# Kernel optimization log

Hardware: AMD Instinct MI355X
Metric: run time of the kernel (lower is better)

Reference implementation:

```python
import jax, jax.numpy as jnp
import numpy as np

E = 1024   # embed_dim
H = 16     # num_heads
D = E // H # head_dim
B = 2
S = 2048
YAT_EPS = 0.1


def setup_inputs() -> dict:
    key = jax.random.key(0)
    ks = jax.random.split(key, 5)
    w_scale = (6.0 / (E + E)) ** 0.5  # xavier_uniform bound
    def xavier(k):
        return jax.random.uniform(k, (E, E), jnp.float32, -w_scale, w_scale)
    return {
        "x": jax.random.normal(ks[0], (B, S, E), jnp.float32),
        "Wq": xavier(ks[1]), "bq": jnp.zeros((E,), jnp.float32),
        "Wk": xavier(ks[2]), "bk": jnp.zeros((E,), jnp.float32),
        "Wv": xavier(ks[3]), "bv": jnp.zeros((E,), jnp.float32),
        "Wo": xavier(ks[4]), "bo": jnp.zeros((E,), jnp.float32),
    }


def reference(x, Wq, bq, Wk, bk, Wv, bv, Wo, bo):
    b, s, _ = x.shape
    # Projections (Linear: x @ W + b, flax kernel layout [in, out])
    Q = x @ Wq + bq
    K = x @ Wk + bk
    V = x @ Wv + bv
    # [B, H, S, D]
    Q = Q.reshape(b, s, H, D).transpose(0, 2, 1, 3)
    K = K.reshape(b, s, H, D).transpose(0, 2, 1, 3)
    V = V.reshape(b, s, H, D).transpose(0, 2, 1, 3)
    # L2 normalize along head_dim
    Qn = Q / (jnp.linalg.norm(Q, axis=-1, keepdims=True) + 1e-8)
    Kn = K / (jnp.linalg.norm(K, axis=-1, keepdims=True) + 1e-8)
    # Yat kernel scores: (1 + <q,k>)^2 / (eps + (1 - <q,k>))
    dot = jnp.einsum("bhqd,bhkd->bhqk", Qn, Kn)
    scores = (1.0 + dot) ** 2 / (YAT_EPS + (1.0 - dot))
    # Sum-normalize (no softmax)
    attn = scores / (jnp.sum(scores, axis=-1, keepdims=True) + 1e-6)
    out = jnp.einsum("bhqk,bhkd->bhqd", attn, V)
    out = out.transpose(0, 2, 1, 3).reshape(b, s, E)
    return out @ Wo + bo
```

## Files before the change

### kernel.cpp

```cpp
#include <hip/hip_runtime.h>
#include <math.h>

#define EDIM 1024
#define NH   16
#define HD   64
#define BATCH 2
#define SEQ  2048
#define NROW (BATCH*SEQ)
#define YAT_EPS 0.1f

typedef _Float16 f16;
typedef _Float16 f16x8 __attribute__((ext_vector_type(8)));
typedef _Float16 f16x4 __attribute__((ext_vector_type(4)));
typedef float    f32x4 __attribute__((ext_vector_type(4)));

#define GLL16(gp, lp) __builtin_amdgcn_global_load_lds( \
    (const __attribute__((address_space(1))) void*)(gp), \
    (__attribute__((address_space(3))) void*)(lp), 16, 0, 0)

__global__ __launch_bounds__(256)
void cast_f16_kernel(const float* __restrict__ src, f16* __restrict__ dst)
{
    const int i = (blockIdx.x * 256 + threadIdx.x) * 4;
    const float4 v = *(const float4*)(src + i);
    f16x4 o = {(f16)v.x, (f16)v.y, (f16)v.z, (f16)v.w};
    *(f16x4*)(dst + i) = o;
}

__global__ __launch_bounds__(256)
void transcast_kernel(const float* __restrict__ W, f16* __restrict__ Wt)
{
    __shared__ float T[32][33];
    const int t = threadIdx.x;
    const int r = t >> 3, c4 = (t & 7) * 4;
    const int bi = blockIdx.x * 32, bj = blockIdx.y * 32;
    const float4 v = *(const float4*)(W + (size_t)(bi + r) * 1024 + bj + c4);
    T[r][c4 + 0] = v.x; T[r][c4 + 1] = v.y; T[r][c4 + 2] = v.z; T[r][c4 + 3] = v.w;
    __syncthreads();
    f16x4 o = {(f16)T[c4 + 0][r], (f16)T[c4 + 1][r], (f16)T[c4 + 2][r], (f16)T[c4 + 3][r]};
    *(f16x4*)(Wt + (size_t)(bj + r) * 1024 + bi + c4) = o;
}

__global__ __launch_bounds__(256)
void gemm_f16(const f16* __restrict__ A,
              const f16* __restrict__ B0, const f16* __restrict__ B1, const f16* __restrict__ B2,
              const float* __restrict__ bi0, const float* __restrict__ bi1, const float* __restrict__ bi2,
              void* __restrict__ o0, void* __restrict__ o1, void* __restrict__ o2,
              int e0, int e1, int e2)
{
    __shared__ __align__(16) f16 As[128 * 64];
    __shared__ __align__(16) f16 Bs[128 * 64];

    const int z = blockIdx.z;
    const f16*   Bt   = (z == 0) ? B0  : (z == 1) ? B1  : B2;
    const float* bias = (z == 0) ? bi0 : (z == 1) ? bi1 : bi2;
    void*        Cout = (z == 0) ? o0  : (z == 1) ? o1  : o2;
    const int    epi  = (z == 0) ? e0  : (z == 1) ? e1  : e2;

    const int tid  = threadIdx.x;
    const int lane = tid & 63;
    const int w    = tid >> 6;
    const int cl   = lane & 15;
    const int quad = lane >> 4;
    const int wm = w & 1, wn = w >> 1;
    const int bm = blockIdx.x * 128, bn = blockIdx.y * 128;

    const int srow = w * 8 + (lane >> 3);
    const int scs  = (lane & 7) ^ (lane >> 3);
    const f16* gA = A  + (size_t)(bm + srow) * 1024 + scs * 8;
    const f16* gB = Bt + (size_t)(bn + srow) * 1024 + scs * 8;
    f16* lA = As + w * 512;
    f16* lB = Bs + w * 512;

    f32x4 acc[4][4];
#pragma unroll
    for (int i = 0; i < 4; ++i)
#pragma unroll
        for (int j = 0; j < 4; ++j) acc[i][j] = (f32x4){0.f, 0.f, 0.f, 0.f};

    for (int k0 = 0; k0 < 1024; k0 += 64) {
        __syncthreads();
#pragma unroll
        for (int it = 0; it < 4; ++it) {
            GLL16(gA + (size_t)it * 32 * 1024 + k0, lA + it * 2048);
            GLL16(gB + (size_t)it * 32 * 1024 + k0, lB + it * 2048);
        }
        __syncthreads();
#pragma unroll
        for (int kb = 0; kb < 2; ++kb) {
            f16x8 af[4], bf[4];
#pragma unroll
            for (int mt = 0; mt < 4; ++mt)
                af[mt] = *(const f16x8*)(&As[(wm * 64 + mt * 16 + cl) * 64 +
                                             (((kb * 4 + quad) ^ (cl & 7)) * 8)]);
#pragma unroll
            for (int nt = 0; nt < 4; ++nt)
                bf[nt] = *(const f16x8*)(&Bs[(wn * 64 + nt * 16 + cl) * 64 +
                                             (((kb * 4 + quad) ^ (cl & 7)) * 8)]);
#pragma unroll
            for (int mt = 0; mt < 4; ++mt)
#pragma unroll
                for (int nt = 0; nt < 4; ++nt)
                    acc[mt][nt] = __builtin_amdgcn_mfma_f32_16x16x32_f16(af[mt], bf[nt], acc[mt][nt], 0, 0, 0);
        }
    }

    float bcol[4];
#pragma unroll
    for (int nt = 0; nt < 4; ++nt) bcol[nt] = bias[bn + wn * 64 + nt * 16 + cl];
#pragma unroll
    for (int mt = 0; mt < 4; ++mt)
#pragma unroll
        for (int nt = 0; nt < 4; ++nt)
#pragma unroll
            for (int rg = 0; rg < 4; ++rg) acc[mt][nt][rg] += bcol[nt];

    if (epi == 0) {
        float* C = (float*)Cout;
#pragma unroll
        for (int mt = 0; mt < 4; ++mt)
#pragma unroll
            for (int rg = 0; rg < 4; ++rg) {
                const int row = bm + wm * 64 + mt * 16 + quad * 4 + rg;
#pragma unroll
                for (int nt = 0; nt < 4; ++nt)
                    C[(size_t)row * EDIM + bn + wn * 64 + nt * 16 + cl] = acc[mt][nt][rg];
            }
    } else if (epi == 1) {
        f16* C = (f16*)Cout;
#pragma unroll
        for (int mt = 0; mt < 4; ++mt)
#pragma unroll
            for (int rg = 0; rg < 4; ++rg) {
                float ss = 0.f;
#pragma unroll
                for (int nt = 0; nt < 4; ++nt) ss += acc[mt][nt][rg] * acc[mt][nt][rg];
                ss += __shfl_xor(ss, 1); ss += __shfl_xor(ss, 2);
                ss += __shfl_xor(ss, 4); ss += __shfl_xor(ss, 8);
                const float inv = 1.0f / (sqrtf(ss) + 1e-8f);
                const int row = bm + wm * 64 + mt * 16 + quad * 4 + rg;
                const int b = row >> 11, s = row & (SEQ - 1);
#pragma unroll
                for (int nt = 0; nt < 4; ++nt) {
                    const int col = bn + wn * 64 + nt * 16 + cl;
                    const int h = col >> 6, d = col & 63;
                    C[((size_t)(b * NH + h) * SEQ + s) * HD + d] = (f16)(acc[mt][nt][rg] * inv);
                }
            }
    } else {
        f16* C = (f16*)Cout;
#pragma unroll
        for (int mt = 0; mt < 4; ++mt) {
            const int s0 = bm + wm * 64 + mt * 16 + quad * 4;
            const int b = s0 >> 11, sl = s0 & (SEQ - 1);
#pragma unroll
            for (int nt = 0; nt < 4; ++nt) {
                const int col = bn + wn * 64 + nt * 16 + cl;
                const int h = col >> 6, d = col & 63;
                f16x4 o = {(f16)acc[mt][nt][0], (f16)acc[mt][nt][1],
                           (f16)acc[mt][nt][2], (f16)acc[mt][nt][3]};
                *(f16x4*)(C + ((size_t)(b * NH + h) * HD + d) * SEQ + sl) = o;
            }
        }
    }
}

__global__ __launch_bounds__(256)
void yat_attn(const f16* __restrict__ Qh, const f16* __restrict__ Kh,
              const f16* __restrict__ Vt, f16* __restrict__ AO)
{
    __shared__ __align__(16) char lds[53248];
    f16* KsB = (f16*)(lds + 20480);
    f16* VsB = (f16*)(lds + 36864);

    const int tid  = threadIdx.x;
    const int lane = tid & 63;
    const int w    = tid >> 6;
    const int cl   = lane & 15;
    const int quad = lane >> 4;
    const int wm = w & 1;
    const int wk = w >> 1;
    const int q0 = blockIdx.x * 128;
    const int bh = blockIdx.y;

    const f16* Qg = Qh + (size_t)bh * SEQ * HD;
    const f16* Kg = Kh + (size_t)bh * SEQ * HD;
    const f16* Vg = Vt + (size_t)bh * HD * SEQ;

    const int g8   = lane >> 3;
    const int scs  = (lane & 7) ^ g8;
    const int qrow = w * 8 + g8;
    const int krow = w * 16 + g8;

    {
        const f16* gQ = Qg + (size_t)(q0 + qrow) * HD + scs * 8;
        f16* lQ = (f16*)lds + w * 512;
#pragma unroll
        for (int it = 0; it < 4; ++it)
            GLL16(gQ + it * 32 * HD, lQ + it * 2048);
    }
    __syncthreads();
    f16x8 qf[4][2];
#pragma unroll
    for (int qt = 0; qt < 4; ++qt)
#pragma unroll
        for (int kb = 0; kb < 2; ++kb)
            qf[qt][kb] = *(const f16x8*)((f16*)lds + (wm * 64 + qt * 16 + cl) * 64 +
                                         ((kb * 4 + quad) ^ (cl & 7)) * 8);
    __syncthreads();

    f16* Pw = (f16*)(lds + w * 5120);

    f32x4 O[4][4];
    float rs[4] = {0.f, 0.f, 0.f, 0.f};
#pragma unroll
    for (int i = 0; i < 4; ++i)
#pragma unroll
        for (int j = 0; j < 4; ++j) O[i][j] = (f32x4){0.f, 0.f, 0.f, 0.f};

    const f16* gK = Kg + (size_t)krow * HD + scs * 8;
    const f16* gV = Vg + (size_t)krow * SEQ + scs * 8;
    f16* lK = KsB + w * 1024;
    f16* lV = VsB + w * 1024;

#pragma unroll
    for (int it = 0; it < 2; ++it) {
        GLL16(gK + (size_t)(it * 8) * HD, lK + it * 512);
        GLL16(gV + (size_t)(it * 8) * SEQ, lV + it * 512);
    }

    for (int t0 = 0; t0 < SEQ; t0 += 64) {
        const int buf = (t0 >> 6) & 1;
        __syncthreads();

        if (t0 + 64 < SEQ) {
            const int nb = buf ^ 1;
#pragma unroll
            for (int it = 0; it < 2; ++it) {
                GLL16(gK + (size_t)(t0 + 64 + it * 8) * HD, lK + nb * 4096 + it * 512);
                GLL16(gV + (size_t)(it * 8) * SEQ + t0 + 64, lV + nb * 4096 + it * 512);
            }
        }

        const f16* Ks = KsB + buf * 4096;
        const f16* Vs = VsB + buf * 4096;

        f32x4 s[2][4];
#pragma unroll
        for (int kt = 0; kt < 2; ++kt)
#pragma unroll
            for (int qt = 0; qt < 4; ++qt) s[kt][qt] = (f32x4){0.f, 0.f, 0.f, 0.f};
#pragma unroll
        for (int kb = 0; kb < 2; ++kb) {
            const int sw = ((kb * 4 + quad) ^ (cl & 7)) * 8;
            f16x8 af0 = *(const f16x8*)(&Ks[(wk * 32 +  0 + cl) * 64 + sw]);
            f16x8 af1 = *(const f16x8*)(&Ks[(wk * 32 + 16 + cl) * 64 + sw]);
#pragma unroll
            for (int qt = 0; qt < 4; ++qt) {
                s[0][qt] = __builtin_amdgcn_mfma_f32_16x16x32_f16(af0, qf[qt][kb], s[0][qt], 0, 0, 0);
                s[1][qt] = __builtin_amdgcn_mfma_f32_16x16x32_f16(af1, qf[qt][kb], s[1][qt], 0, 0, 0);
            }
        }

#pragma unroll
        for (int kt = 0; kt < 2; ++kt)
#pragma unroll
            for (int qt = 0; qt < 4; ++qt) {
                f16x4 pk;
                float psum = 0.f;
#pragma unroll
                for (int rg = 0; rg < 4; ++rg) {
                    const float u = (1.0f + YAT_EPS) - s[kt][qt][rg];
                    const float p = fmaf(4.41f, __builtin_amdgcn_rcpf(u), u - 4.2f);
                    psum += p;
                    pk[rg] = (f16)p;
                }
                rs[qt] += psum;
                *(f16x4*)(&Pw[(qt * 16 + cl) * 40 + kt * 16 + quad * 4]) = pk;
            }

        f16x8 pa[4];
#pragma unroll
        for (int qt = 0; qt < 4; ++qt)
            pa[qt] = *(const f16x8*)(&Pw[(qt * 16 + cl) * 40 + quad * 8]);
#pragma unroll
        for (int dn = 0; dn < 4; ++dn) {
            f16x8 vb = *(const f16x8*)(&Vs[(dn * 16 + cl) * 64 +
                                           ((wk * 4 + quad) ^ (cl & 7)) * 8]);
#pragma unroll
            for (int qt = 0; qt < 4; ++qt)
                O[qt][dn] = __builtin_amdgcn_mfma_f32_16x16x32_f16(pa[qt], vb, O[qt][dn], 0, 0, 0);
        }
    }

    __syncthreads();
    float* rs_s = (float*)lds;
    float* Ox   = (float*)(lds + 20480);

#pragma unroll
    for (int qt = 0; qt < 4; ++qt) {
        float t = rs[qt];
        t += __shfl_xor(t, 16);
        t += __shfl_xor(t, 32);
        if (quad == 0) rs_s[wk * 128 + wm * 64 + qt * 16 + cl] = t;
    }
    if (wk == 1) {
#pragma unroll
        for (int qt = 0; qt < 4; ++qt)
#pragma unroll
            for (int dn = 0; dn < 4; ++dn)
#pragma unroll
                for (int rg = 0; rg < 4; ++rg)
                    Ox[(wm * 64 + qt * 16 + quad * 4 + rg) * 64 + dn * 16 + cl] = O[qt][dn][rg];
    }
    __syncthreads();
    if (wk == 0) {
        const int b = bh >> 4, h = bh & 15;
#pragma unroll
        for (int qt = 0; qt < 4; ++qt)
#pragma unroll
            for (int rg = 0; rg < 4; ++rg) {
                const int ql = wm * 64 + qt * 16 + quad * 4 + rg;
                const float tot = rs_s[ql] + rs_s[128 + ql];
                const float inv = 1.0f / (tot + 1e-6f);
                const size_t rowoff = ((size_t)b * SEQ + q0 + ql) * EDIM + h * 64;
#pragma unroll
                for (int dn = 0; dn < 4; ++dn)
                    AO[rowoff + dn * 16 + cl] =
                        (f16)((O[qt][dn][rg] + Ox[ql * 64 + dn * 16 + cl]) * inv);
            }
    }
}

extern "C" void kernel_launch(void* const* d_in, const int* in_sizes, int n_in,
                              void* d_out, int out_size, void* d_ws, size_t ws_size,
                              hipStream_t stream)
{
    const float* x  = (const float*)d_in[0];
    const float* Wq = (const float*)d_in[1];
    const float* bq = (const float*)d_in[2];
    const float* Wk = (const float*)d_in[3];
    const float* bk = (const float*)d_in[4];
    const float* Wv = (const float*)d_in[5];
    const float* bv = (const float*)d_in[6];
    const float* Wo = (const float*)d_in[7];
    const float* bo = (const float*)d_in[8];

    char* p = (char*)d_ws;
    f16* xb  = (f16*)p;                 p += (size_t)NROW * EDIM * 2;
    f16* Wqt = (f16*)p;                 p += (size_t)EDIM * EDIM * 2;
    f16* Wkt = (f16*)p;                 p += (size_t)EDIM * EDIM * 2;
    f16* Wvt = (f16*)p;                 p += (size_t)EDIM * EDIM * 2;
    f16* Wot = (f16*)p;                 p += (size_t)EDIM * EDIM * 2;
    f16* Qhb = (f16*)p;                 p += (size_t)NROW * EDIM * 2;
    f16* Khb = (f16*)p;                 p += (size_t)NROW * EDIM * 2;
    f16* Vtb = (f16*)p;                 p += (size_t)NROW * EDIM * 2;
    f16* AOb = (f16*)p;                 p += (size_t)NROW * EDIM * 2;

    cast_f16_kernel<<<NROW * EDIM / 1024, 256, 0, stream>>>(x, xb);
    transcast_kernel<<<dim3(32, 32), 256, 0, stream>>>(Wq, Wqt);
    transcast_kernel<<<dim3(32, 32), 256, 0, stream>>>(Wk, Wkt);
    transcast_kernel<<<dim3(32, 32), 256, 0, stream>>>(Wv, Wvt);
    transcast_kernel<<<dim3(32, 32), 256, 0, stream>>>(Wo, Wot);

    gemm_f16<<<dim3(NROW / 128, EDIM / 128, 3), 256, 0, stream>>>(
        xb, Wqt, Wkt, Wvt, bq, bk, bv, Qhb, Khb, Vtb, 1, 1, 2);

    yat_attn<<<dim3(SEQ / 128, BATCH * NH), 256, 0, stream>>>(Qhb, Khb, Vtb, AOb);

    gemm_f16<<<dim3(NROW / 128, EDIM / 128, 1), 256, 0, stream>>>(
        AOb, Wot, Wot, Wot, bo, bo, bo, d_out, d_out, d_out, 0, 0, 0);
}
```

Before: 210.7 us.

## Double-buffer GEMM with 64x128 tiles, LDS-staged epilogue stores, merged weight transposes

```diff
diff --git a/kernel.cpp b/kernel.cpp
--- a/kernel.cpp
+++ b/kernel.cpp
@@ -28,8 +28,15 @@
 }
 
 __global__ __launch_bounds__(256)
-void transcast_kernel(const float* __restrict__ W, f16* __restrict__ Wt)
+void transcast4_kernel(const float* __restrict__ W0, const float* __restrict__ W1,
+                       const float* __restrict__ W2, const float* __restrict__ W3,
+                       f16* __restrict__ T0, f16* __restrict__ T1,
+                       f16* __restrict__ T2, f16* __restrict__ T3)
 {
+    const int z = blockIdx.z;
+    const float* W = (z == 0) ? W0 : (z == 1) ? W1 : (z == 2) ? W2 : W3;
+    f16*         Wt = (z == 0) ? T0 : (z == 1) ? T1 : (z == 2) ? T2 : T3;
+
     __shared__ float T[32][33];
     const int t = threadIdx.x;
     const int r = t >> 3, c4 = (t & 7) * 4;
@@ -48,8 +55,7 @@
               void* __restrict__ o0, void* __restrict__ o1, void* __restrict__ o2,
               int e0, int e1, int e2)
 {
-    __shared__ __align__(16) f16 As[128 * 64];
-    __shared__ __align__(16) f16 Bs[128 * 64];
+    __shared__ __align__(16) char lds[24576];
 
     const int z = blockIdx.z;
     const f16*   Bt   = (z == 0) ? B0  : (z == 1) ? B1  : B2;
@@ -63,73 +69,83 @@
     const int cl   = lane & 15;
     const int quad = lane >> 4;
     const int wm = w & 1, wn = w >> 1;
-    const int bm = blockIdx.x * 128, bn = blockIdx.y * 128;
-
-    const int srow = w * 8 + (lane >> 3);
-    const int scs  = (lane & 7) ^ (lane >> 3);
-    const f16* gA = A  + (size_t)(bm + srow) * 1024 + scs * 8;
-    const f16* gB = Bt + (size_t)(bn + srow) * 1024 + scs * 8;
+    const int bm = blockIdx.x * 64, bn = blockIdx.y * 128;
+
+    f16* As = (f16*)lds;
+    f16* Bs = (f16*)(lds + 8192);
+
+    const int srow = lane >> 2;
+    const int scs  = (lane & 3) ^ (srow & 3);
+    const f16* gA = A  + (size_t)(bm + w * 16 + srow) * 1024 + scs * 8;
+    const f16* gB = Bt + (size_t)(bn + w * 32 + srow) * 1024 + scs * 8;
     f16* lA = As + w * 512;
-    f16* lB = Bs + w * 512;
-
-    f32x4 acc[4][4];
-#pragma unroll
-    for (int i = 0; i < 4; ++i)
+    f16* lB = Bs + w * 1024;
+
+    f32x4 acc[2][4];
+#pragma unroll
+    for (int i = 0; i < 2; ++i)
 #pragma unroll
         for (int j = 0; j < 4; ++j) acc[i][j] = (f32x4){0.f, 0.f, 0.f, 0.f};
 
-    for (int k0 = 0; k0 < 1024; k0 += 64) {
-        __syncthreads();
-#pragma unroll
-        for (int it = 0; it < 4; ++it) {
-            GLL16(gA + (size_t)it * 32 * 1024 + k0, lA + it * 2048);
-            GLL16(gB + (size_t)it * 32 * 1024 + k0, lB + it * 2048);
-        }
-        __syncthreads();
-#pragma unroll
-        for (int kb = 0; kb < 2; ++kb) {
-            f16x8 af[4], bf[4];
-#pragma unroll
-            for (int mt = 0; mt < 4; ++mt)
-                af[mt] = *(const f16x8*)(&As[(wm * 64 + mt * 16 + cl) * 64 +
-                                             (((kb * 4 + quad) ^ (cl & 7)) * 8)]);
+    GLL16(gA, lA);
+    GLL16(gB, lB);
+    GLL16(gB + 16 * 1024, lB + 512);
+
+    const int fsw = (quad ^ (cl & 3)) * 8;
+
+    for (int it = 0; it < 32; ++it) {
+        const int buf = it & 1;
+        __syncthreads();
+        if (it < 31) {
+            const int k0 = (it + 1) * 32;
+            const int nb = buf ^ 1;
+            GLL16(gA + k0, lA + nb * 2048);
+            GLL16(gB + k0, lB + nb * 4096);
+            GLL16(gB + 16 * 1024 + k0, lB + nb * 4096 + 512);
+        }
+        f16x8 af[2], bf[4];
+#pragma unroll
+        for (int mt = 0; mt < 2; ++mt)
+            af[mt] = *(const f16x8*)(&As[buf * 2048 + (wm * 32 + mt * 16 + cl) * 32 + fsw]);
+#pragma unroll
+        for (int nt = 0; nt < 4; ++nt)
+            bf[nt] = *(const f16x8*)(&Bs[buf * 4096 + (wn * 64 + nt * 16 + cl) * 32 + fsw]);
+#pragma unroll
+        for (int mt = 0; mt < 2; ++mt)
 #pragma unroll
             for (int nt = 0; nt < 4; ++nt)
-                bf[nt] = *(const f16x8*)(&Bs[(wn * 64 + nt * 16 + cl) * 64 +
-                                             (((kb * 4 + quad) ^ (cl & 7)) * 8)]);
-#pragma unroll
-            for (int mt = 0; mt < 4; ++mt)
-#pragma unroll
-                for (int nt = 0; nt < 4; ++nt)
-                    acc[mt][nt] = __builtin_amdgcn_mfma_f32_16x16x32_f16(af[mt], bf[nt], acc[mt][nt], 0, 0, 0);
-        }
+                acc[mt][nt] = __builtin_amdgcn_mfma_f32_16x16x32_f16(af[mt], bf[nt], acc[mt][nt], 0, 0, 0);
     }
 
     float bcol[4];
 #pragma unroll
     for (int nt = 0; nt < 4; ++nt) bcol[nt] = bias[bn + wn * 64 + nt * 16 + cl];
 #pragma unroll
-    for (int mt = 0; mt < 4; ++mt)
+    for (int mt = 0; mt < 2; ++mt)
 #pragma unroll
         for (int nt = 0; nt < 4; ++nt)
 #pragma unroll
             for (int rg = 0; rg < 4; ++rg) acc[mt][nt][rg] += bcol[nt];
+
+    const int b_idx = bm >> 11, sl0 = bm & (SEQ - 1), h0 = bn >> 6;
 
     if (epi == 0) {
         float* C = (float*)Cout;
 #pragma unroll
-        for (int mt = 0; mt < 4; ++mt)
+        for (int mt = 0; mt < 2; ++mt)
 #pragma unroll
             for (int rg = 0; rg < 4; ++rg) {
-                const int row = bm + wm * 64 + mt * 16 + quad * 4 + rg;
+                const int row = bm + wm * 32 + mt * 16 + quad * 4 + rg;
 #pragma unroll
                 for (int nt = 0; nt < 4; ++nt)
                     C[(size_t)row * EDIM + bn + wn * 64 + nt * 16 + cl] = acc[mt][nt][rg];
             }
     } else if (epi == 1) {
         f16* C = (f16*)Cout;
-#pragma unroll
-        for (int mt = 0; mt < 4; ++mt)
+        __syncthreads();
+        f16* S = (f16*)lds;
+#pragma unroll
+        for (int mt = 0; mt < 2; ++mt)
 #pragma unroll
             for (int rg = 0; rg < 4; ++rg) {
                 float ss = 0.f;
@@ -138,29 +154,46 @@
                 ss += __shfl_xor(ss, 1); ss += __shfl_xor(ss, 2);
                 ss += __shfl_xor(ss, 4); ss += __shfl_xor(ss, 8);
                 const float inv = 1.0f / (sqrtf(ss) + 1e-8f);
-                const int row = bm + wm * 64 + mt * 16 + quad * 4 + rg;
-                const int b = row >> 11, s = row & (SEQ - 1);
+                const int row = wm * 32 + mt * 16 + quad * 4 + rg;
 #pragma unroll
                 for (int nt = 0; nt < 4; ++nt) {
-                    const int col = bn + wn * 64 + nt * 16 + cl;
-                    const int h = col >> 6, d = col & 63;
-                    C[((size_t)(b * NH + h) * SEQ + s) * HD + d] = (f16)(acc[mt][nt][rg] * inv);
+                    const int col = wn * 64 + nt * 16 + cl;
+                    S[row * 128 + (((col >> 3) ^ (row & 15)) * 8) + (col & 7)] =
+                        (f16)(acc[mt][nt][rg] * inv);
                 }
             }
+        __syncthreads();
+#pragma unroll
+        for (int i = 0; i < 4; ++i) {
+            const int c = tid + i * 256;
+            const int s = c >> 4, gi = c & 15;
+            f16x8 v = *(const f16x8*)(&S[s * 128 + ((gi ^ (s & 15)) * 8)]);
+            const int head = h0 + (gi >> 3), d8 = (gi & 7) * 8;
+            *(f16x8*)(C + ((size_t)(b_idx * NH + head) * SEQ + sl0 + s) * HD + d8) = v;
+        }
     } else {
         f16* C = (f16*)Cout;
-#pragma unroll
-        for (int mt = 0; mt < 4; ++mt) {
-            const int s0 = bm + wm * 64 + mt * 16 + quad * 4;
-            const int b = s0 >> 11, sl = s0 & (SEQ - 1);
+        __syncthreads();
+        f16* S = (f16*)lds;
+#pragma unroll
+        for (int mt = 0; mt < 2; ++mt) {
+            const int s0 = wm * 32 + mt * 16 + quad * 4;
 #pragma unroll
             for (int nt = 0; nt < 4; ++nt) {
-                const int col = bn + wn * 64 + nt * 16 + cl;
-                const int h = col >> 6, d = col & 63;
+                const int col = wn * 64 + nt * 16 + cl;
                 f16x4 o = {(f16)acc[mt][nt][0], (f16)acc[mt][nt][1],
                            (f16)acc[mt][nt][2], (f16)acc[mt][nt][3]};
-                *(f16x4*)(C + ((size_t)(b * NH + h) * HD + d) * SEQ + sl) = o;
-            }
+                *(f16x4*)(&S[col * 64 + (((s0 >> 3) ^ (col & 7)) * 8) + (s0 & 7)]) = o;
+            }
+        }
+        __syncthreads();
+#pragma unroll
+        for (int i = 0; i < 4; ++i) {
+            const int c = tid + i * 256;
+            const int col = c >> 3, gi = c & 7;
+            f16x8 v = *(const f16x8*)(&S[col * 64 + ((gi ^ (col & 7)) * 8)]);
+            const int head = h0 + (col >> 6), d = col & 63;
+            *(f16x8*)(C + ((size_t)(b_idx * NH + head) * HD + d) * SEQ + sl0 + gi * 8) = v;
         }
     }
 }
@@ -358,16 +391,14 @@
     f16* AOb = (f16*)p;                 p += (size_t)NROW * EDIM * 2;
 
     cast_f16_kernel<<<NROW * EDIM / 1024, 256, 0, stream>>>(x, xb);
-    transcast_kernel<<<dim3(32, 32), 256, 0, stream>>>(Wq, Wqt);
-    transcast_kernel<<<dim3(32, 32), 256, 0, stream>>>(Wk, Wkt);
-    transcast_kernel<<<dim3(32, 32), 256, 0, stream>>>(Wv, Wvt);
-    transcast_kernel<<<dim3(32, 32), 256, 0, stream>>>(Wo, Wot);
-
-    gemm_f16<<<dim3(NROW / 128, EDIM / 128, 3), 256, 0, stream>>>(
+    transcast4_kernel<<<dim3(32, 32, 4), 256, 0, stream>>>(Wq, Wk, Wv, Wo,
+                                                           Wqt, Wkt, Wvt, Wot);
+
+    gemm_f16<<<dim3(NROW / 64, EDIM / 128, 3), 256, 0, stream>>>(
         xb, Wqt, Wkt, Wvt, bq, bk, bv, Qhb, Khb, Vtb, 1, 1, 2);
 
     yat_attn<<<dim3(SEQ / 128, BATCH * NH), 256, 0, stream>>>(Qhb, Khb, Vtb, AOb);
 
-    gemm_f16<<<dim3(NROW / 128, EDIM / 128, 1), 256, 0, stream>>>(
+    gemm_f16<<<dim3(NROW / 64, EDIM / 128, 1), 256, 0, stream>>>(
         AOb, Wot, Wot, Wot, bo, bo, bo, d_out, d_out, d_out, 0, 0, 0);
 }
```

Result: no change. 211.7 us (+0.5%).
